# Kernel tuning notes

Hardware: AMD Instinct MI355X
Metric: run time of the kernel (lower is better)

The kernel has to match this reference:

```python
import jax, jax.numpy as jnp
import numpy as np

B, S, D_IN, D_OUT = 4, 2048, 4096, 4096


def setup_inputs() -> dict:
    key = jax.random.key(0)
    k1, k2, k3 = jax.random.split(key, 3)
    # int32 activations (already quantized upstream in the original pipeline)
    x_i32 = jax.random.randint(k1, (B, S, D_IN), -128, 128, dtype=jnp.int32)
    # int8 weights in [in, out] layout (Linear weight transposed), symmetric range [-127, 127]
    weight_i8 = jax.random.randint(k2, (D_IN, D_OUT), -127, 128, dtype=jnp.int32).astype(jnp.int8)
    # bias quantized affine to int32 (scale=16 in original)
    bias_i32 = jax.random.randint(k3, (D_OUT,), -2048, 2048, dtype=jnp.int32)
    return {"x_i32": x_i32, "weight_i8": weight_i8, "bias_i32": bias_i32, "out_shift": 7}


def reference(x_i32, weight_i8, bias_i32, out_shift):
    x_shape = x_i32.shape
    x2d = x_i32.reshape(-1, x_shape[-1]).astype(jnp.int32)  # [tokens, d_in]
    # int8 weights upcast to int32, plain int32 matmul with int32 accumulation
    y = jnp.matmul(x2d, weight_i8.astype(jnp.int32), preferred_element_type=jnp.int32)
    y = y + bias_i32  # fused bias add (int32)
    if out_shift > 0:  # out_shift is a static Python int
        y = jnp.right_shift(y, out_shift)  # arithmetic shift on signed int32
    return y.reshape(*x_shape[:-1], y.shape[-1]).astype(jnp.int32)
```

## Files before the change

kernel.cpp:

```cpp
#include <hip/hip_runtime.h>

using int32x4 = __attribute__((ext_vector_type(4))) int;

#define BM 256
#define BN 256
#define TBUF 32768

__global__ __launch_bounds__(256) void pack_x_kernel(const int32x4* __restrict__ x,
                                                     int32x4* __restrict__ xp,
                                                     int nvec) {
    int t = blockIdx.x * 256 + threadIdx.x;
    if (t >= nvec) return;
    int32x4 a = x[t * 4 + 0];
    int32x4 b = x[t * 4 + 1];
    int32x4 c = x[t * 4 + 2];
    int32x4 d = x[t * 4 + 3];
    int32x4 o;
    o.x = (a.x & 255) | ((a.y & 255) << 8) | ((a.z & 255) << 16) | (a.w << 24);
    o.y = (b.x & 255) | ((b.y & 255) << 8) | ((b.z & 255) << 16) | (b.w << 24);
    o.z = (c.x & 255) | ((c.y & 255) << 8) | ((c.z & 255) << 16) | (c.w << 24);
    o.w = (d.x & 255) | ((d.y & 255) << 8) | ((d.z & 255) << 16) | (d.w << 24);
    xp[t] = o;
}

__global__ __launch_bounds__(256) void transform_w_kernel(const int* __restrict__ w,
                                                          unsigned char* __restrict__ wt,
                                                          int K, int N) {
    __shared__ unsigned char tileT[64][72];
    int tx = threadIdx.x & 15;
    int ty = threadIdx.x >> 4;
    int n0 = blockIdx.x * 64;
    int k0 = blockIdx.y * 64;
#pragma unroll
    for (int r = 0; r < 4; ++r) {
        int row = ty * 4 + r;
        int32x4 v = *(const int32x4*)&w[(size_t)(k0 + row) * N + n0 + tx * 4];
        tileT[tx * 4 + 0][row] = (unsigned char)(v.x & 255);
        tileT[tx * 4 + 1][row] = (unsigned char)(v.y & 255);
        tileT[tx * 4 + 2][row] = (unsigned char)(v.z & 255);
        tileT[tx * 4 + 3][row] = (unsigned char)(v.w & 255);
    }
    __syncthreads();
#pragma unroll
    for (int r = 0; r < 4; ++r) {
        int row = ty * 4 + r;
        uchar4 v = *(const uchar4*)&tileT[row][tx * 4];
        *(uchar4*)&wt[(size_t)(n0 + row) * K + k0 + tx * 4] = v;
    }
}

__global__ __launch_bounds__(512, 2) void gemm_i8_1b(
    const char* __restrict__ A,
    const char* __restrict__ Bt,
    const int* __restrict__ bias,
    const int* __restrict__ shiftp,
    int* __restrict__ C,
    int M, int N, int K) {
    __shared__ char smem[4 * TBUF];

    const int nbn = N / BN;
    const int nwg = gridDim.x;
    const int bid = blockIdx.x;
    const int cpx = nwg >> 3;
    const int swz = (bid & 7) * cpx + (bid >> 3);
    const int m0 = (swz / nbn) * BM;
    const int n0 = (swz % nbn) * BN;

    const int t = threadIdx.x;
    const int lane = t & 63;
    const int wave = t >> 6;
    const int wr = wave >> 2;
    const int wc = wave & 3;

    const int s_row = t >> 2;
    const int s_col = ((t & 3) << 4) ^ (((t >> 3) & 3) << 4);
    const char* a_src = A + (size_t)(m0 + s_row) * K + s_col;
    const char* b_src = Bt + (size_t)(n0 + s_row) * K + s_col;
    const size_t jstr = (size_t)128 * K;
    char* lds_st = smem + t * 16;

    const int lr = lane & 15;
    const int lc = (lane >> 4) << 4;
    const int xr = ((lr >> 1) & 3) << 4;
    const int a_off = ((wr << 7) + lr) * 64 + (lc ^ xr);
    const int b_off = 16384 + ((wc << 6) + lr) * 64 + (lc ^ xr);

    int32x4 acc[8][4] = {};
    int32x4 afX[4], afY[4], bfX[4], bfY[4];

    const int nt = K / 64;

#define GLL(src, dst)                                                 \
    __builtin_amdgcn_global_load_lds(                                 \
        (const __attribute__((address_space(1))) void*)(src),        \
        (__attribute__((address_space(3))) void*)(dst), 16, 0, 0)

#define FENCE asm volatile("" ::: "memory")
#define BARR                           \
    do {                               \
        FENCE;                         \
        __builtin_amdgcn_s_barrier();  \
        FENCE;                         \
    } while (0)
#define SB0 __builtin_amdgcn_sched_barrier(0)
#define LGKM0                                                   \
    do {                                                        \
        asm volatile("s_waitcnt lgkmcnt(0)" ::: "memory");      \
        SB0;                                                    \
    } while (0)
#define VMW(n)                                                  \
    do {                                                        \
        asm volatile("s_waitcnt vmcnt(" #n ")" ::: "memory");   \
        SB0;                                                    \
    } while (0)

#define TILE(TT, BFC, BFN, DOSTAGE, DOREADN, WTAIL)                                    \
    do {                                                                               \
        const int base_ = ((TT) & 3) * TBUF;                                           \
        const int nbase_ = (((TT) + 1) & 3) * TBUF;                                    \
        const int sb_ = (((TT) + 3) & 3) * TBUF;                                       \
        const size_t kc_ = (size_t)((TT) + 3) * 64;                                    \
        BARR;                                                                          \
        _Pragma("unroll") for (int i = 0; i < 4; ++i)                                  \
            afY[i] = *(const int32x4*)&smem[base_ + a_off + (4 + i) * 1024];           \
        if (DOSTAGE) {                                                                 \
            GLL(a_src + kc_, lds_st + sb_);                                            \
            GLL(a_src + jstr + kc_, lds_st + sb_ + 8192);                              \
        }                                                                              \
        SB0;                                                                           \
        __builtin_amdgcn_s_setprio(1);                                                 \
        _Pragma("unroll") for (int mi = 0; mi < 4; ++mi)                               \
            _Pragma("unroll") for (int ni = 0; ni < 4; ++ni)                           \
                acc[mi][ni] = __builtin_amdgcn_mfma_i32_16x16x64_i8(                   \
                    afX[mi], BFC[ni], acc[mi][ni], 0, 0, 0);                           \
        __builtin_amdgcn_s_setprio(0);                                                 \
        LGKM0;                                           \
        if (DOREADN) {                                                                 \
            _Pragma("unroll") for (int i = 0; i < 4; ++i)                              \
                afX[i] = *(const int32x4*)&smem[nbase_ + a_off + i * 1024];            \
            _Pragma("unroll") for (int i = 0; i < 4; ++i)                              \
                BFN[i] = *(const int32x4*)&smem[nbase_ + b_off + i * 1024];            \
        }                                                                              \
        if (DOSTAGE) {                                                                 \
            GLL(b_src + kc_, lds_st + sb_ + 16384);                                    \
            GLL(b_src + jstr + kc_, lds_st + sb_ + 24576);                             \
        }                                                                              \
        SB0;                                                                           \
        __builtin_amdgcn_s_setprio(1);                                                 \
        _Pragma("unroll") for (int mi = 0; mi < 4; ++mi)                               \
            _Pragma("unroll") for (int ni = 0; ni < 4; ++ni)                           \
                acc[4 + mi][ni] = __builtin_amdgcn_mfma_i32_16x16x64_i8(               \
                    afY[mi], BFC[ni], acc[4 + mi][ni], 0, 0, 0);                       \
        __builtin_amdgcn_s_setprio(0);                                                 \
        if (DOREADN) LGKM0;                           \
        WTAIL;                                                                         \
    } while (0)

#pragma unroll
    for (int p = 0; p < 3; ++p) {
        GLL(a_src + p * 64, lds_st + p * TBUF);
        GLL(a_src + jstr + p * 64, lds_st + p * TBUF + 8192);
        GLL(b_src + p * 64, lds_st + p * TBUF + 16384);
        GLL(b_src + jstr + p * 64, lds_st + p * TBUF + 24576);
    }
    VMW(8);
    BARR;
#pragma unroll
    for (int i = 0; i < 4; ++i) afX[i] = *(const int32x4*)&smem[a_off + i * 1024];
#pragma unroll
    for (int i = 0; i < 4; ++i) bfX[i] = *(const int32x4*)&smem[b_off + i * 1024];
    LGKM0;
    VMW(4);

    int tt = 0;
    for (; tt < nt - 4; tt += 2) {
        TILE(tt, bfX, bfY, 1, 1, VMW(4));
        TILE(tt + 1, bfY, bfX, 1, 1, VMW(4));
    }
    TILE(nt - 4, bfX, bfY, 1, 1, VMW(4));
    TILE(nt - 3, bfY, bfX, 0, 1, VMW(0));
    TILE(nt - 2, bfX, bfY, 0, 1, (void)0);
    TILE(nt - 1, bfY, bfX, 0, 0, (void)0);

    const int s = *shiftp;
    const int crow = (lane >> 4) << 2;
    const int ccol = lane & 15;
    int bv[4];
#pragma unroll
    for (int nf = 0; nf < 4; ++nf) bv[nf] = bias[n0 + wc * 64 + nf * 16 + ccol];
#pragma unroll
    for (int mf = 0; mf < 8; ++mf) {
        const int grow0 = m0 + wr * 128 + mf * 16 + crow;
#pragma unroll
        for (int nf = 0; nf < 4; ++nf) {
            const int gcol = n0 + wc * 64 + nf * 16 + ccol;
#pragma unroll
            for (int r = 0; r < 4; ++r) {
                int y = acc[mf][nf][r] + bv[nf];
                y = (s > 0) ? (y >> s) : y;
                C[(size_t)(grow0 + r) * N + gcol] = y;
            }
        }
    }
#undef GLL
#undef FENCE
#undef BARR
#undef SB0
#undef LGKM0
#undef VMW
#undef TILE
}

extern "C" void kernel_launch(void* const* d_in, const int* in_sizes, int n_in,
                              void* d_out, int out_size, void* d_ws, size_t ws_size,
                              hipStream_t stream) {
    const int* x = (const int*)d_in[0];
    const int* w = (const int*)d_in[1];
    const int* bias = (const int*)d_in[2];
    const int* shiftp = (const int*)d_in[3];
    int* out = (int*)d_out;

    const int N = in_sizes[2];
    const int K = in_sizes[1] / N;
    const int M = in_sizes[0] / K;

    char* xp = (char*)d_ws;
    unsigned char* wt = (unsigned char*)d_ws + (size_t)M * K;

    int nvec = (int)(((long long)M * K) / 16);
    pack_x_kernel<<<(nvec + 255) / 256, 256, 0, stream>>>((const int32x4*)x, (int32x4*)xp, nvec);

    dim3 tgrid(N / 64, K / 64);
    transform_w_kernel<<<tgrid, 256, 0, stream>>>(w, wt, K, N);

    int nwg = (M / BM) * (N / BN);
    gemm_i8_1b<<<nwg, 512, 0, stream>>>(xp, (const char*)wt, bias, shiftp, out, M, N, K);
}
```

Before: 182.6 us.

## Load B fragments directly from global memory into registers, bypassing LDS

The B (weight) operand is no longer staged through LDS. Each wave loads its B fragments straight from global memory into registers one tile ahead, and LDS now holds only the A tiles, halving shared memory per block. The barrier moves to the end of each tile and the vmcnt waits are retuned. This removes LDS traffic and capacity for B, but the 4 waves sharing a column now each fetch the same B data from global/L2, and those loads have only one tile of latency hiding.

New measurement: 249.8 us. +36.8%, slower.

```diff
diff --git a/kernel.cpp b/kernel.cpp
--- a/kernel.cpp
+++ b/kernel.cpp
@@ -4,7 +4,7 @@
 
 #define BM 256
 #define BN 256
-#define TBUF 32768
+#define ABUF 16384
 
 __global__ __launch_bounds__(256) void pack_x_kernel(const int32x4* __restrict__ x,
                                                      int32x4* __restrict__ xp,
@@ -49,14 +49,14 @@
     }
 }
 
-__global__ __launch_bounds__(512, 2) void gemm_i8_1b(
+__global__ __launch_bounds__(512, 2) void gemm_i8_bg(
     const char* __restrict__ A,
     const char* __restrict__ Bt,
     const int* __restrict__ bias,
     const int* __restrict__ shiftp,
     int* __restrict__ C,
     int M, int N, int K) {
-    __shared__ char smem[4 * TBUF];
+    __shared__ char smem[4 * ABUF];
 
     const int nbn = N / BN;
     const int nwg = gridDim.x;
@@ -75,7 +75,6 @@
     const int s_row = t >> 2;
     const int s_col = ((t & 3) << 4) ^ (((t >> 3) & 3) << 4);
     const char* a_src = A + (size_t)(m0 + s_row) * K + s_col;
-    const char* b_src = Bt + (size_t)(n0 + s_row) * K + s_col;
     const size_t jstr = (size_t)128 * K;
     char* lds_st = smem + t * 16;
 
@@ -83,7 +82,9 @@
     const int lc = (lane >> 4) << 4;
     const int xr = ((lr >> 1) & 3) << 4;
     const int a_off = ((wr << 7) + lr) * 64 + (lc ^ xr);
-    const int b_off = 16384 + ((wc << 6) + lr) * 64 + (lc ^ xr);
+
+    const char* b_base = Bt + (size_t)(n0 + (wc << 6) + lr) * K + lc;
+    const size_t n16 = (size_t)16 * K;
 
     int32x4 acc[8][4] = {};
     int32x4 afX[4], afY[4], bfX[4], bfY[4];
@@ -114,18 +115,22 @@
         SB0;                                                    \
     } while (0)
 
-#define TILE(TT, BFC, BFN, DOSTAGE, DOREADN, WTAIL)                                    \
+#define TILE(TT, BFC, BFN, DOSTAGE, DOLOADB, DOREADN, WTAIL, DOBARR)                   \
     do {                                                                               \
-        const int base_ = ((TT) & 3) * TBUF;                                           \
-        const int nbase_ = (((TT) + 1) & 3) * TBUF;                                    \
-        const int sb_ = (((TT) + 3) & 3) * TBUF;                                       \
-        const size_t kc_ = (size_t)((TT) + 3) * 64;                                    \
-        BARR;                                                                          \
+        const int base_ = ((TT) & 3) * ABUF;                                           \
+        const int nbase_ = (((TT) + 1) & 3) * ABUF;                                    \
+        const int sb_ = (((TT) + 3) & 3) * ABUF;                                       \
+        const size_t kg_ = (size_t)((TT) + 3) * 64;                                    \
+        const size_t kb_ = (size_t)((TT) + 1) * 64;                                    \
         _Pragma("unroll") for (int i = 0; i < 4; ++i)                                  \
             afY[i] = *(const int32x4*)&smem[base_ + a_off + (4 + i) * 1024];           \
+        if (DOLOADB) {                                                                 \
+            _Pragma("unroll") for (int nf = 0; nf < 4; ++nf)                           \
+                BFN[nf] = *(const int32x4*)(b_base + nf * n16 + kb_);                  \
+        }                                                                              \
         if (DOSTAGE) {                                                                 \
-            GLL(a_src + kc_, lds_st + sb_);                                            \
-            GLL(a_src + jstr + kc_, lds_st + sb_ + 8192);                              \
+            GLL(a_src + kg_, lds_st + sb_);                                            \
+            GLL(a_src + jstr + kg_, lds_st + sb_ + 8192);                              \
         }                                                                              \
         SB0;                                                                           \
         __builtin_amdgcn_s_setprio(1);                                                 \
@@ -138,12 +143,6 @@
         if (DOREADN) {                                                                 \
             _Pragma("unroll") for (int i = 0; i < 4; ++i)                              \
                 afX[i] = *(const int32x4*)&smem[nbase_ + a_off + i * 1024];            \
-            _Pragma("unroll") for (int i = 0; i < 4; ++i)                              \
-                BFN[i] = *(const int32x4*)&smem[nbase_ + b_off + i * 1024];            \
-        }                                                                              \
-        if (DOSTAGE) {                                                                 \
-            GLL(b_src + kc_, lds_st + sb_ + 16384);                                    \
-            GLL(b_src + jstr + kc_, lds_st + sb_ + 24576);                             \
         }                                                                              \
         SB0;                                                                           \
         __builtin_amdgcn_s_setprio(1);                                                 \
@@ -152,35 +151,33 @@
                 acc[4 + mi][ni] = __builtin_amdgcn_mfma_i32_16x16x64_i8(               \
                     afY[mi], BFC[ni], acc[4 + mi][ni], 0, 0, 0);                       \
         __builtin_amdgcn_s_setprio(0);                                                 \
-        if (DOREADN) LGKM0;                           \
+        if (DOREADN) LGKM0;                         \
         WTAIL;                                                                         \
+        if (DOBARR) BARR;                                                              \
     } while (0)
 
 #pragma unroll
     for (int p = 0; p < 3; ++p) {
-        GLL(a_src + p * 64, lds_st + p * TBUF);
-        GLL(a_src + jstr + p * 64, lds_st + p * TBUF + 8192);
-        GLL(b_src + p * 64, lds_st + p * TBUF + 16384);
-        GLL(b_src + jstr + p * 64, lds_st + p * TBUF + 24576);
-    }
-    VMW(8);
+        GLL(a_src + p * 64, lds_st + p * ABUF);
+        GLL(a_src + jstr + p * 64, lds_st + p * ABUF + 8192);
+    }
+#pragma unroll
+    for (int nf = 0; nf < 4; ++nf) bfX[nf] = *(const int32x4*)(b_base + nf * n16);
+    VMW(0);
     BARR;
 #pragma unroll
     for (int i = 0; i < 4; ++i) afX[i] = *(const int32x4*)&smem[a_off + i * 1024];
-#pragma unroll
-    for (int i = 0; i < 4; ++i) bfX[i] = *(const int32x4*)&smem[b_off + i * 1024];
     LGKM0;
-    VMW(4);
 
     int tt = 0;
     for (; tt < nt - 4; tt += 2) {
-        TILE(tt, bfX, bfY, 1, 1, VMW(4));
-        TILE(tt + 1, bfY, bfX, 1, 1, VMW(4));
-    }
-    TILE(nt - 4, bfX, bfY, 1, 1, VMW(4));
-    TILE(nt - 3, bfY, bfX, 0, 1, VMW(0));
-    TILE(nt - 2, bfX, bfY, 0, 1, (void)0);
-    TILE(nt - 1, bfY, bfX, 0, 0, (void)0);
+        TILE(tt, bfX, bfY, 1, 1, 1, VMW(2), 1);
+        TILE(tt + 1, bfY, bfX, 1, 1, 1, VMW(2), 1);
+    }
+    TILE(nt - 4, bfX, bfY, 1, 1, 1, VMW(2), 1);
+    TILE(nt - 3, bfY, bfX, 0, 1, 1, VMW(0), 1);
+    TILE(nt - 2, bfX, bfY, 0, 1, 1, VMW(0), 1);
+    TILE(nt - 1, bfY, bfX, 0, 0, 0, (void)0, 0);
 
     const int s = *shiftp;
     const int crow = (lane >> 4) << 2;
@@ -234,5 +231,5 @@
     transform_w_kernel<<<tgrid, 256, 0, stream>>>(w, wt, K, N);
 
     int nwg = (M / BM) * (N / BN);
-    gemm_i8_1b<<<nwg, 512, 0, stream>>>(xp, (const char*)wt, bias, shiftp, out, M, N, K);
-}
+    gemm_i8_bg<<<nwg, 512, 0, stream>>>(xp, (const char*)wt, bias, shiftp, out, M, N, K);
+}
```
